# Kernel optimization log

Hardware: AMD Instinct MI355X
Metric: run time of the kernel (lower is better)

The kernel has to match this reference:

```python
import jax, jax.numpy as jnp
import numpy as np

# nqsystems=8 grouped sites, physical dim d=2^ncontraq=16,
# state bond r=64, layer (unitary MPO) bond rl=16, operator MPO bond ro=4,
# nlsystems=1 pre-contracted circuit layer.
NQ, R, D, RL, RO, NL = 8, 64, 16, 16, 4, 1


def setup_inputs() -> dict:
    key = jax.random.key(0)
    k1, k2, k3 = jax.random.split(key, 3)
    # scale so contractions stay O(1) numerically
    state = jax.random.normal(k1, (NQ, R, D, R), jnp.float32) / np.float32(np.sqrt(R * D))
    layer = jax.random.normal(k2, (NL, NQ, RL, D, D, RL), jnp.float32) / np.float32(np.sqrt(RL * D))
    operator = jax.random.normal(k3, (NQ, RO, D, D, RO), jnp.float32) / np.float32(np.sqrt(RO * D))
    return {"state": state, "layer": layer, "operator": operator}


def reference(state, layer, operator):
    """<psi| U^dagger O U |psi> contracted site-by-site along the TT chain.

    state:    [nq, r, d, r]        TT cores of |psi>
    layer:    [nl, nq, rl, d, d, rl]  TT-operator cores of the circuit layer (nl=1)
    operator: [nq, ro, d, d, ro]   TT-operator cores of the observable
    """
    r, rl, ro = state.shape[1], layer.shape[3], operator.shape[1]
    # open-boundary closure: boundary vectors = e0 on every bond
    env0 = jnp.zeros((r, rl, ro, rl, r), state.dtype).at[0, 0, 0, 0, 0].set(1.0)
    U = layer[0]  # nlsystems == 1

    def step(env, cores):
        S, Uq, Oq = cores
        # tt_dagger: conj + transpose physical indices (0,2,1,3)
        Ud = jnp.conj(Uq).transpose(0, 2, 1, 3)
        # env axes: a=bra-state bond, l=bra-layer bond, o=operator bond,
        #           m=ket-layer bond, b=ket-state bond
        t = jnp.einsum('alomb,aiA->lombiA', env, jnp.conj(S))   # bra state core
        t = jnp.einsum('lombiA,lijL->ombAjL', t, Ud)            # U^dagger core
        t = jnp.einsum('ombAjL,ojkO->mbALkO', t, Oq)            # observable core
        t = jnp.einsum('mbALkO,mksM->bALOsM', t, Uq)            # U core
        t = jnp.einsum('bALOsM,bsB->ALOMB', t, S)               # ket state core
        return t, None

    env, _ = jax.lax.scan(step, env0, (state, U, operator))
    return env[0, 0, 0, 0, 0]
```

## Files before the change

kernel.cpp:

```cpp
#include <hip/hip_runtime.h>


typedef __attribute__((ext_vector_type(8))) short bf16x8;
typedef __attribute__((ext_vector_type(8))) _Float16 f16x8;
typedef __attribute__((ext_vector_type(4))) float f32x4;
typedef __attribute__((ext_vector_type(4))) unsigned short us4;

static __device__ __forceinline__ unsigned short f2bf(float x) {
    union { float f; unsigned u; } a; a.f = x;
    return (unsigned short)((a.u + 0x7FFF + ((a.u >> 16) & 1)) >> 16);
}
static __device__ __forceinline__ float bf2f(unsigned short h) {
    union { unsigned u; float f; } a; a.u = (unsigned)h << 16; return a.f;
}
static __device__ __forceinline__ unsigned split2(float x) {
    unsigned short h = f2bf(x);
    unsigned short l = f2bf(x - bf2f(h));
    return (unsigned)h | ((unsigned)l << 16);
}
static __device__ __forceinline__ void split2_pair(float x0, float x1,
                                                   unsigned& o0, unsigned& o1) {
    unsigned hh, ll;
    asm("v_cvt_pk_bf16_f32 %0, %1, %2" : "=v"(hh) : "v"(x0), "v"(x1));
    union { unsigned u; float f; } c0, c1;
    c0.u = hh << 16;
    c1.u = hh & 0xffff0000u;
    float r0 = x0 - c0.f, r1 = x1 - c1.f;
    asm("v_cvt_pk_bf16_f32 %0, %1, %2" : "=v"(ll) : "v"(r0), "v"(r1));
    asm("v_perm_b32 %0, %1, %2, %3" : "=v"(o0) : "v"(ll), "v"(hh), "s"(0x05040100));
    asm("v_perm_b32 %0, %1, %2, %3" : "=v"(o1) : "v"(ll), "v"(hh), "s"(0x07060302));
}
static __device__ __forceinline__ unsigned short f2h_bits(float x) {
    union { _Float16 h; unsigned short u; } c; c.h = (_Float16)x; return c.u;
}
static __device__ __forceinline__ float h2f_bits(unsigned short u) {
    union { unsigned short u; _Float16 h; } c; c.u = u; return (float)c.h;
}
static __device__ __forceinline__ void gl_lds16(const unsigned short* g,
                                                unsigned short* l) {
    __builtin_amdgcn_global_load_lds(
        (const __attribute__((address_space(1))) unsigned int*)g,
        (__attribute__((address_space(3))) unsigned int*)l, 16, 0, 0);
}

__global__ void write_diag_kernel(float* out, float v) {
    if (threadIdx.x == 0 && blockIdx.x == 0) out[0] = v;
}
__global__ void zero_out(float* o) {
    if (threadIdx.x == 0 && blockIdx.x == 0) o[0] = 0.0f;
}

__global__ void prep_apack(const float* __restrict__ layer,
                           unsigned short* __restrict__ Ap2,
                           unsigned short* __restrict__ Ap4) {
    int idx = blockIdx.x * 256 + threadIdx.x;
    int q = idx >> 13, k0 = (idx >> 10) & 7, mt = (idx >> 6) & 15, lane = idx & 63;
    int quad = lane >> 4, r = lane & 15;
    unsigned short h2[8], l2[8], h4[8], l4[8];
#pragma unroll
    for (int j = 0; j < 8; j++) {
        int k = k0 * 32 + quad * 8 + j;
        int m = mt * 16 + r;
        float v2 = layer[(size_t)q * 65536 +
                         (size_t)((((k >> 4) * 16 + (m >> 4)) * 16 + (k & 15)) * 16 + (m & 15))];
        float v4 = layer[(size_t)q * 65536 +
                         (size_t)((((k >> 4) * 16 + (k & 15)) * 16 + (m >> 4)) * 16 + (m & 15))];
        h2[j] = f2h_bits(v2); l2[j] = f2h_bits(v2 - h2f_bits(h2[j]));
        h4[j] = f2h_bits(v4); l4[j] = f2h_bits(v4 - h2f_bits(h4[j]));
    }
    size_t base = ((size_t)((q * 8 + k0) * 16 + mt) * 2) * 512 + lane * 8;
    *(us4*)(Ap2 + base)       = *(us4*)&h2[0];
    *(us4*)(Ap2 + base + 4)   = *(us4*)&h2[4];
    *(us4*)(Ap2 + base + 512) = *(us4*)&l2[0];
    *(us4*)(Ap2 + base + 516) = *(us4*)&l2[4];
    *(us4*)(Ap4 + base)       = *(us4*)&h4[0];
    *(us4*)(Ap4 + base + 4)   = *(us4*)&h4[4];
    *(us4*)(Ap4 + base + 512) = *(us4*)&l4[0];
    *(us4*)(Ap4 + base + 516) = *(us4*)&l4[4];
}

__global__ void prep_spack1(const float* __restrict__ state,
                            unsigned short* __restrict__ Sp1) {
    int idx = blockIdx.x * 256 + threadIdx.x;
    int q = idx >> 13, c = (idx >> 11) & 3, k0 = (idx >> 10) & 1,
        mt = (idx >> 6) & 15, lane = idx & 63;
    int quad = lane >> 4, lr = lane & 15;
    unsigned short h[8], l[8];
#pragma unroll
    for (int j = 0; j < 8; j++) {
        int k = k0 * 32 + quad * 8 + j;
        float v = state[(size_t)q * 65536 + (size_t)(k * 16 + mt) * 64 + c * 16 + lr];
        h[j] = f2bf(v); l[j] = f2bf(v - bf2f(h[j]));
    }
    size_t base = (size_t)(q * 4 + c) * 32768 + ((size_t)(k0 * 16 + mt) * 2) * 512 + lane * 8;
    *(us4*)(Sp1 + base)       = *(us4*)&h[0];
    *(us4*)(Sp1 + base + 4)   = *(us4*)&h[4];
    *(us4*)(Sp1 + base + 512) = *(us4*)&l[0];
    *(us4*)(Sp1 + base + 516) = *(us4*)&l[4];
}

__global__ void prep_spack5(const float* __restrict__ state,
                            unsigned short* __restrict__ Sp5) {
    int idx = blockIdx.x * 256 + threadIdx.x;
    int q = idx >> 13, k0 = (idx >> 8) & 31, mt = (idx >> 6) & 3, lane = idx & 63;
    int quad = lane >> 4, lr = lane & 15;
    unsigned short h[8], l[8];
#pragma unroll
    for (int j = 0; j < 8; j++) {
        int k = k0 * 32 + quad * 8 + j;
        int s = k >> 6, b = k & 63;
        float v = state[(size_t)q * 65536 + (size_t)(b * 16 + s) * 64 + mt * 16 + lr];
        h[j] = f2bf(v); l[j] = f2bf(v - bf2f(h[j]));
    }
    size_t base = (size_t)q * 131072 + ((size_t)(k0 * 4 + mt) * 2) * 512 + lane * 8;
    *(us4*)(Sp5 + base)       = *(us4*)&h[0];
    *(us4*)(Sp5 + base + 4)   = *(us4*)&h[4];
    *(us4*)(Sp5 + base + 512) = *(us4*)&l[0];
    *(us4*)(Sp5 + base + 516) = *(us4*)&l[4];
}

__global__ void prep_opack3(const float* __restrict__ oper,
                            unsigned short* __restrict__ Op3) {
    int idx = blockIdx.x * 256 + threadIdx.x;
    int q = idx >> 9, k0 = (idx >> 8) & 1, mt = (idx >> 6) & 3, lane = idx & 63;
    int quad = lane >> 4, lr = lane & 15;
    unsigned short h[8], l[8];
#pragma unroll
    for (int j = 0; j < 8; j++) {
        int k = k0 * 32 + quad * 8 + j;
        int m = mt * 16 + lr;
        float v = oper[(size_t)q * 4096 + (size_t)(k * 16 + (m & 15)) * 4 + (m >> 4)];
        h[j] = f2h_bits(v); l[j] = f2h_bits(v - h2f_bits(h[j]));
    }
    size_t base = (size_t)q * 8192 + ((size_t)(k0 * 4 + mt) * 2) * 512 + lane * 8;
    *(us4*)(Op3 + base)       = *(us4*)&h[0];
    *(us4*)(Op3 + base + 4)   = *(us4*)&h[4];
    *(us4*)(Op3 + base + 512) = *(us4*)&l[0];
    *(us4*)(Op3 + base + 516) = *(us4*)&l[4];
}

__global__ void env_split_k(const float* __restrict__ env, unsigned* __restrict__ envS) {
    int t = blockIdx.x * 256 + threadIdx.x;
    float4 v = ((const float4*)env)[t];
    uint4 o;
    o.x = split2(v.x); o.y = split2(v.y); o.z = split2(v.z); o.w = split2(v.w);
    ((uint4*)envS)[t] = o;
}

__global__ void s0_g2(const float* __restrict__ state, const float* __restrict__ layer,
                      float* __restrict__ g2) {
    int t = blockIdx.x * 256 + threadIdx.x;
    int A = t >> 8, j = (t >> 4) & 15, L = t & 15;
    float s = 0;
    for (int i = 0; i < 16; i++) s += state[i * 64 + A] * layer[(j * 16 + i) * 16 + L];
    g2[t] = s;
}
__global__ void s0_g3(const float* __restrict__ g2, const float* __restrict__ oper,
                      float* __restrict__ g3) {
    int t = blockIdx.x * 256 + threadIdx.x;
    int A = t >> 10, L = (t >> 6) & 15, k = (t >> 2) & 15, O = t & 3;
    float s = 0;
    for (int j = 0; j < 16; j++) s += g2[A * 256 + j * 16 + L] * oper[(j * 16 + k) * 4 + O];
    g3[t] = s;
}
__global__ void s0_g4(const float* __restrict__ g3, const float* __restrict__ layer,
                      float* __restrict__ g4) {
    int t = blockIdx.x * 256 + threadIdx.x;
    int A = t >> 14, L = (t >> 10) & 15, O = (t >> 8) & 3, sp = (t >> 4) & 15, M = t & 15;
    float s = 0;
    for (int k = 0; k < 16; k++)
        s += g3[A * 1024 + L * 64 + k * 4 + O] * layer[(k * 16 + sp) * 16 + M];
    g4[t] = s;
}
__global__ void s0_env(const float* __restrict__ g4, const float* __restrict__ state,
                       float* __restrict__ env) {
    int t = blockIdx.x * 256 + threadIdx.x;
    int A = t >> 16, L = (t >> 12) & 15, O = (t >> 10) & 3, M = (t >> 6) & 15, B = t & 63;
    float s = 0;
    for (int sp = 0; sp < 16; sp++)
        s += g4[A * 16384 + L * 1024 + O * 256 + sp * 16 + M] * state[sp * 64 + B];
    env[(size_t)(L * 64 + O * 16 + M) * 4096 + A * 64 + B] = s;
}

__global__ void s7_c1(const float* __restrict__ state, const float* __restrict__ layer,
                      float* __restrict__ c1) {
    int t = blockIdx.x * 256 + threadIdx.x;
    int l = t >> 10, a = (t >> 4) & 63, j = t & 15;
    float s = 0;
    for (int i = 0; i < 16; i++)
        s += state[7 * 65536 + (a * 16 + i) * 64] * layer[7 * 65536 + ((l * 16 + j) * 16 + i) * 16];
    c1[t] = s;
}
__global__ void s7_c2(const float* __restrict__ c1, const float* __restrict__ oper,
                      float* __restrict__ c2) {
    int t = blockIdx.x * 256 + threadIdx.x;
    int o = t >> 14, l = (t >> 10) & 15, a = (t >> 4) & 63, k = t & 15;
    float s = 0;
    for (int j = 0; j < 16; j++)
        s += c1[l * 1024 + a * 16 + j] * oper[7 * 4096 + ((o * 16 + j) * 16 + k) * 4];
    c2[t] = s;
}
__global__ void s7_c3(const float* __restrict__ c2, const float* __restrict__ layer,
                      float* __restrict__ c3) {
    int t = blockIdx.x * 256 + threadIdx.x;
    int m = t >> 16, o = (t >> 14) & 3, l = (t >> 10) & 15, a = (t >> 4) & 63, sp = t & 15;
    float s = 0;
    for (int k = 0; k < 16; k++)
        s += c2[o * 16384 + l * 1024 + a * 16 + k] *
             layer[7 * 65536 + ((m * 16 + k) * 16 + sp) * 16];
    c3[t] = s;
}
__global__ void prep_sv(const float* __restrict__ state, float* __restrict__ sv) {
    int t = blockIdx.x * 256 + threadIdx.x;
    sv[t] = state[7 * 65536 + t * 64];
}
__global__ __launch_bounds__(256) void s7_fused(const float* __restrict__ env,
                                                const float* __restrict__ c3,
                                                const float* __restrict__ sv,
                                                float* __restrict__ out) {
    __shared__ float c3s[1024], svs[1024], red[256];
    int t = threadIdx.x;
    int n0 = blockIdx.x * 64;
    int l = n0 >> 12, o = (n0 >> 10) & 3, m = (n0 >> 6) & 15;
    const float* c3b = c3 + m * 65536 + o * 16384 + l * 1024;
    const float* eb  = env + (size_t)blockIdx.x * 4096;
    for (int i = t; i < 1024; i += 256) { c3s[i] = c3b[i]; svs[i] = sv[i]; }
    __syncthreads();
    float s = 0;
    int b = t & 63, ag = t >> 6;
#pragma unroll
    for (int g = 0; g < 16; g++) {
        int a = ag * 16 + g;
        float e = eb[a * 64 + b];
        float w = 0;
#pragma unroll
        for (int sp = 0; sp < 16; sp++) w += c3s[a * 16 + sp] * svs[b * 16 + sp];
        s += e * w;
    }
    red[t] = s; __syncthreads();
    for (int off = 128; off; off >>= 1) { if (t < off) red[t] += red[t + off]; __syncthreads(); }
    if (t == 0) atomicAdd(out, red[0]);
}

static __device__ __forceinline__ void g1_body(int bid, void* smem,
                                               const unsigned* __restrict__ envS,
                                               const unsigned short* __restrict__ Sp1,
                                               unsigned short* __restrict__ t1,
                                               float scale) {
    unsigned* Bt = (unsigned*)smem;
    const int tid = threadIdx.x, lane = tid & 63, wave = tid >> 6;
    const int quad = lane >> 4, lr = lane & 15;
    const int cc = bid >> 10, rid = bid & 1023;
    const int l = rid >> 6, o = (rid >> 4) & 3, m2 = rid & 15;

    f32x4 acc[4][4];
#pragma unroll
    for (int i = 0; i < 4; i++)
#pragma unroll
        for (int j = 0; j < 4; j++)
#pragma unroll
            for (int r = 0; r < 4; r++) acc[i][j][r] = 0.0f;

    const unsigned* Bv = envS + (size_t)rid * 4096;
    const unsigned short* Sp1c = Sp1 + (size_t)cc * 32768;
    uint4 ur[2];
    auto load_tile = [&](int k0) {
        const uint4* src = (const uint4*)(Bv + k0 * 2048);
        ur[0] = src[tid];
        ur[1] = src[256 + tid];
    };
    auto store_tile = [&]() {
#pragma unroll
        for (int v = 0; v < 2; v++) {
            int e = v * 256 + tid;
            unsigned* p = &Bt[(e >> 4) * 65 + (e & 15) * 4];
            p[0] = ur[v].x; p[1] = ur[v].y; p[2] = ur[v].z; p[3] = ur[v].w;
        }
    };

    bf16x8 ahb[2][4], alb[2][4];
    auto loadA = [&](int k0, int buf) {
#pragma unroll
        for (int mt = 0; mt < 4; mt++) {
            int gmt = wave * 4 + mt;
            const unsigned short* ap = Sp1c + ((size_t)(k0 * 16 + gmt) * 2) * 512 + lane * 8;
            ahb[buf][mt] = *(const bf16x8*)ap;
            alb[buf][mt] = *(const bf16x8*)(ap + 512);
        }
    };

    load_tile(0);
    loadA(0, 0);
    store_tile();
#pragma unroll
    for (int k0 = 0; k0 < 2; k0++) {
        __syncthreads();
        if (k0 + 1 < 2) { load_tile(k0 + 1); loadA(k0 + 1, 1); }
#pragma unroll
        for (int nt = 0; nt < 4; nt++) {
            int nl = nt * 16 + lr;
            bf16x8 bh, bl;
#pragma unroll
            for (int j = 0; j < 8; j++) {
                unsigned u = Bt[(quad * 8 + j) * 65 + nl];
                bh[j] = (short)(u & 0xffffu);
                bl[j] = (short)(u >> 16);
            }
#pragma unroll
            for (int mt = 0; mt < 4; mt++) {
                acc[mt][nt] = __builtin_amdgcn_mfma_f32_16x16x32_bf16(ahb[k0][mt], bh, acc[mt][nt], 0, 0, 0);
                acc[mt][nt] = __builtin_amdgcn_mfma_f32_16x16x32_bf16(ahb[k0][mt], bl, acc[mt][nt], 0, 0, 0);
                acc[mt][nt] = __builtin_amdgcn_mfma_f32_16x16x32_bf16(alb[k0][mt], bh, acc[mt][nt], 0, 0, 0);
            }
        }
        __syncthreads();
        if (k0 + 1 < 2) store_tile();
    }

#pragma unroll
    for (int nt = 0; nt < 4; nt++) {
        int b = nt * 16 + lr;
#pragma unroll
        for (int r = 0; r < 4; r++) {
            int a4 = quad * 4 + r;
            us4 w;
#pragma unroll
            for (int mt = 0; mt < 4; mt++) w[mt] = f2h_bits(acc[mt][nt][r] * scale);
            size_t addr = (size_t)cc * 16777216 +
                          (size_t)(o * 256 + m2 * 16 + a4) * 16384 +
                          (size_t)(l * 2 + (wave >> 1)) * 512 + b * 8 + (wave & 1) * 4;
            *(us4*)(t1 + addr) = w;
        }
    }
}

__global__ __launch_bounds__(256) void gemm_g1(const unsigned* __restrict__ envS,
                                               const unsigned short* __restrict__ Sp1,
                                               unsigned short* __restrict__ t1,
                                               float scale) {
    __shared__ unsigned Bt[32 * 65];
    g1_body(blockIdx.x, Bt, envS, Sp1, t1, scale);
}

static __device__ __forceinline__ void g2_body(int bid, void* smem,
                                               const unsigned short* __restrict__ Bp,
                                               const unsigned short* __restrict__ Ap,
                                               unsigned short* __restrict__ Co) {
    unsigned short* Bs = (unsigned short*)smem;
    const int tid = threadIdx.x, lane = tid & 63, wave = tid >> 6;
    const int quad = lane >> 4, lr = lane & 15;
    const int cc = bid >> 10, rid = bid & 1023;
    const int o = rid >> 8, m2 = (rid >> 4) & 15, a4 = rid & 15;
    const unsigned short* pb = Bp + (size_t)bid * 16384;
    unsigned short* Cb = Co + (size_t)cc * 16777216;

#pragma unroll
    for (int i = 0; i < 8; i++)
        gl_lds16(pb + i * 2048 + tid * 8, Bs + i * 2048 + wave * 512);

    f32x4 acc[4][4];
#pragma unroll
    for (int i = 0; i < 4; i++)
#pragma unroll
        for (int j = 0; j < 4; j++)
#pragma unroll
            for (int r = 0; r < 4; r++) acc[i][j][r] = 0.0f;

    f16x8 ah[3][4];
    auto loadA = [&](int k0, int buf) {
#pragma unroll
        for (int mt = 0; mt < 4; mt++) {
            int gmt = wave * 4 + mt;
            ah[buf][mt] = *(const f16x8*)(Ap + ((size_t)(k0 * 16 + gmt) * 2) * 512 + lane * 8);
        }
    };
    loadA(0, 0);
    loadA(1, 1);

    asm volatile("s_waitcnt vmcnt(0)" ::: "memory");
    __syncthreads();

#pragma unroll
    for (int k0 = 0; k0 < 8; k0++) {
        if (k0 + 2 < 8) loadA(k0 + 2, (k0 + 2) % 3);
        f16x8 bfr[4];
#pragma unroll
        for (int nt = 0; nt < 4; nt++)
            bfr[nt] = *(const f16x8*)(Bs + (k0 * 4 + quad) * 512 + (nt * 16 + lr) * 8);
#pragma unroll
        for (int nt = 0; nt < 4; nt++)
#pragma unroll
            for (int mt = 0; mt < 4; mt++)
                acc[mt][nt] = __builtin_amdgcn_mfma_f32_16x16x32_f16(
                    ah[k0 % 3][mt], bfr[nt], acc[mt][nt], 0, 0, 0);
    }

#pragma unroll
    for (int nt = 0; nt < 4; nt++) {
        int b = nt * 16 + lr;
#pragma unroll
        for (int r = 0; r < 4; r++) {
            int L = quad * 4 + r;
            us4 w;
#pragma unroll
            for (int mt = 0; mt < 4; mt++) w[mt] = f2h_bits(acc[mt][nt][r]);
            size_t addr = (size_t)(L * 256 + m2 * 16 + a4) * 4096 +
                          (size_t)(o * 2 + (wave >> 1)) * 512 + b * 8 + (wave & 1) * 4;
            *(us4*)(Cb + addr) = w;
        }
    }
}

__global__ __launch_bounds__(256) void gemm_g2(const unsigned short* __restrict__ Bp,
                                               const unsigned short* __restrict__ Ap,
                                               unsigned short* __restrict__ Co) {
    __shared__ __align__(16) unsigned short Bs[16384];
    g2_body(blockIdx.x, Bs, Bp, Ap, Co);
}

__global__ __launch_bounds__(256) void gemm_g45(const unsigned short* __restrict__ T2,
                                                const unsigned short* __restrict__ Op3q,
                                                const unsigned short* __restrict__ Ap4,
                                                const unsigned short* __restrict__ Sp5,
                                                float* __restrict__ env,
                                                unsigned* __restrict__ envSo,
                                                int A0, float inv, int wf32) {
    __shared__ __align__(16) unsigned short Bs[16384];
    __shared__ unsigned SL[4 * 16 * 68];
    const int tid = threadIdx.x, lane = tid & 63, wave = tid >> 6;
    const int quad = lane >> 4, lr = lane & 15;
    const int cc = blockIdx.x >> 10, rid = blockIdx.x & 1023;
    const int low = rid & 7, O2 = (rid >> 3) & 3, g = rid >> 5;
    const int panel = g * 8 + low;
    const int L = panel >> 4, a4 = panel & 15;
    const unsigned short* T2c = T2 + (size_t)cc * 16777216;
    const int b8 = (wave * 16 + lr) * 8;

    f16x8 ah[3][4];
    auto loadA = [&](int k0, int buf) {
#pragma unroll
        for (int mt = 0; mt < 4; mt++) {
            int gmt = wave * 4 + mt;
            ah[buf][mt] = *(const f16x8*)(Ap4 + ((size_t)(k0 * 16 + gmt) * 2) * 512 + lane * 8);
        }
    };
    loadA(0, 0);
    loadA(1, 1);

    {
        f16x8 oh0 = *(const f16x8*)(Op3q + (size_t)(O2 * 2) * 512 + lane * 8);
        f16x8 oh1 = *(const f16x8*)(Op3q + (size_t)((4 + O2) * 2) * 512 + lane * 8);
        f16x8 tb[5][2];
        auto loadT2 = [&](int m2, int buf) {
            const unsigned short* pp = T2c + (size_t)(L * 256 + m2 * 16 + a4) * 4096;
            tb[buf][0] = *(const f16x8*)(pp + (quad << 9) + b8);
            tb[buf][1] = *(const f16x8*)(pp + ((4 + quad) << 9) + b8);
        };
        loadT2(0, 0); loadT2(1, 1); loadT2(2, 2); loadT2(3, 3);
#pragma unroll
        for (int m2 = 0; m2 < 16; m2++) {
            if (m2 + 4 < 16) loadT2(m2 + 4, (m2 + 4) % 5);
            f32x4 a3;
            a3[0] = a3[1] = a3[2] = a3[3] = 0.0f;
            a3 = __builtin_amdgcn_mfma_f32_16x16x32_f16(oh0, tb[m2 % 5][0], a3, 0, 0, 0);
            a3 = __builtin_amdgcn_mfma_f32_16x16x32_f16(oh1, tb[m2 % 5][1], a3, 0, 0, 0);
            us4 w;
#pragma unroll
            for (int r = 0; r < 4; r++) w[r] = f2h_bits(a3[r]);
            *(us4*)(Bs + (m2 * 2 + (quad >> 1)) * 512 + b8 + (quad & 1) * 4) = w;
        }
    }
    __syncthreads();

    f32x4 acc[4][4];
#pragma unroll
    for (int i = 0; i < 4; i++)
#pragma unroll
        for (int j = 0; j < 4; j++)
#pragma unroll
            for (int r = 0; r < 4; r++) acc[i][j][r] = 0.0f;

#pragma unroll
    for (int k0 = 0; k0 < 8; k0++) {
        if (k0 + 2 < 8) loadA(k0 + 2, (k0 + 2) % 3);
        f16x8 bfr[4];
#pragma unroll
        for (int nt = 0; nt < 4; nt++)
            bfr[nt] = *(const f16x8*)(Bs + (k0 * 4 + quad) * 512 + (nt * 16 + lr) * 8);
#pragma unroll
        for (int nt = 0; nt < 4; nt++)
#pragma unroll
            for (int mt = 0; mt < 4; mt++)
                acc[mt][nt] = __builtin_amdgcn_mfma_f32_16x16x32_f16(
                    ah[k0 % 3][mt], bfr[nt], acc[mt][nt], 0, 0, 0);
    }

    unsigned* myslab = SL + wave * (16 * 68);
    f32x4 acc5[4];
#pragma unroll
    for (int nt = 0; nt < 4; nt++)
#pragma unroll
        for (int r = 0; r < 4; r++) acc5[nt][r] = 0.0f;

    bf16x8 s5h[2][4], s5l[2][4];
    auto loadS5 = [&](int step, int buf) {
        int kg = (wave * 4 + (step >> 1)) * 2 + (step & 1);
#pragma unroll
        for (int nt = 0; nt < 4; nt++) {
            const unsigned short* bp = Sp5 + ((size_t)(kg * 4 + nt) * 2) * 512 + lane * 8;
            s5h[buf][nt] = *(const bf16x8*)bp;
            s5l[buf][nt] = *(const bf16x8*)(bp + 512);
        }
    };
    loadS5(0, 0);

#pragma unroll
    for (int mtp = 0; mtp < 4; mtp++) {
#pragma unroll
        for (int nt = 0; nt < 4; nt++) {
            unsigned o0, o1, o2, o3;
            split2_pair(acc[mtp][nt][0], acc[mtp][nt][1], o0, o1);
            split2_pair(acc[mtp][nt][2], acc[mtp][nt][3], o2, o3);
            myslab[(quad * 4 + 0) * 68 + nt * 16 + lr] = o0;
            myslab[(quad * 4 + 1) * 68 + nt * 16 + lr] = o1;
            myslab[(quad * 4 + 2) * 68 + nt * 16 + lr] = o2;
            myslab[(quad * 4 + 3) * 68 + nt * 16 + lr] = o3;
        }
        asm volatile("s_waitcnt lgkmcnt(0)" ::: "memory");
#pragma unroll
        for (int h = 0; h < 2; h++) {
            const int step = mtp * 2 + h;
            const unsigned* sp = &myslab[lr * 68 + h * 32 + quad * 8];
            uint4 u0 = *(const uint4*)sp;
            uint4 u1 = *(const uint4*)(sp + 4);
            bf16x8 th, tl;
            th[0] = (short)(u0.x & 0xffff); tl[0] = (short)(u0.x >> 16);
            th[1] = (short)(u0.y & 0xffff); tl[1] = (short)(u0.y >> 16);
            th[2] = (short)(u0.z & 0xffff); tl[2] = (short)(u0.z >> 16);
            th[3] = (short)(u0.w & 0xffff); tl[3] = (short)(u0.w >> 16);
            th[4] = (short)(u1.x & 0xffff); tl[4] = (short)(u1.x >> 16);
            th[5] = (short)(u1.y & 0xffff); tl[5] = (short)(u1.y >> 16);
            th[6] = (short)(u1.z & 0xffff); tl[6] = (short)(u1.z >> 16);
            th[7] = (short)(u1.w & 0xffff); tl[7] = (short)(u1.w >> 16);
            if (step + 1 < 8) loadS5(step + 1, (step + 1) & 1);
#pragma unroll
            for (int nt = 0; nt < 4; nt++) {
                acc5[nt] = __builtin_amdgcn_mfma_f32_16x16x32_bf16(th, s5h[step & 1][nt], acc5[nt], 0, 0, 0);
                acc5[nt] = __builtin_amdgcn_mfma_f32_16x16x32_bf16(th, s5l[step & 1][nt], acc5[nt], 0, 0, 0);
                acc5[nt] = __builtin_amdgcn_mfma_f32_16x16x32_bf16(tl, s5h[step & 1][nt], acc5[nt], 0, 0, 0);
            }
        }
    }

    __syncthreads();
    float* red = (float*)SL;
#pragma unroll
    for (int nt = 0; nt < 4; nt++)
#pragma unroll
        for (int r = 0; r < 4; r++)
            red[wave * 1088 + (quad * 4 + r) * 68 + nt * 16 + lr] = acc5[nt][r];
    __syncthreads();
    float wv[4];
#pragma unroll
    for (int r = 0; r < 4; r++) {
        int M2 = quad * 4 + r, Bc = wave * 16 + lr;
        float v = red[M2 * 68 + Bc] + red[1088 + M2 * 68 + Bc] +
                  red[2176 + M2 * 68 + Bc] + red[3264 + M2 * 68 + Bc];
        wv[r] = v * inv;
    }
    unsigned s0p, s1p, s2p, s3p;
    split2_pair(wv[0], wv[1], s0p, s1p);
    split2_pair(wv[2], wv[3], s2p, s3p);
    unsigned sp4[4] = {s0p, s1p, s2p, s3p};
#pragma unroll
    for (int r = 0; r < 4; r++) {
        int M2 = quad * 4 + r, Bc = wave * 16 + lr;
        size_t idx = (size_t)(L * 64 + O2 * 16 + M2) * 4096 + (A0 + cc * 16 + a4) * 64 + Bc;
        envSo[idx] = sp4[r];
        if (wf32) env[idx] = wv[r];
    }
}

__global__ __launch_bounds__(256) void fused_g2_g1(
        const unsigned short* __restrict__ Bp,
        const unsigned short* __restrict__ Ap,
        unsigned short* __restrict__ Co,
        const unsigned* __restrict__ envS,
        const unsigned short* __restrict__ Sp1b,
        unsigned short* __restrict__ t1,
        float scale) {
    __shared__ __align__(16) unsigned char smem[32768];
    const int grp = blockIdx.x >> 3;
    const int sub = (grp >> 1) * 8 + (blockIdx.x & 7);
    if (grp & 1)
        g1_body(sub, smem, envS, Sp1b, t1, scale);
    else
        g2_body(sub, smem, Bp, Ap, Co);
}

extern "C" void kernel_launch(void* const* d_in, const int* in_sizes, int n_in,
                              void* d_out, int out_size, void* d_ws, size_t ws_size,
                              hipStream_t stream) {
    const float* state = (const float*)d_in[0];
    const float* layer = (const float*)d_in[1];
    const float* oper  = (const float*)d_in[2];
    float* out = (float*)d_out;

    const size_t need = 16777216ull * 4 + 33554432ull * 4 + 3ull * 4194304ull * 4 +
                        (4ull * 1048576ull + 65536ull) * 2ull + 4096ull;
    if (ws_size < need) {
        write_diag_kernel<<<1, 64, 0, stream>>>(out, (float)ws_size);
        return;
    }
    float* F    = (float*)d_ws;
    unsigned* P = (unsigned*)(F + 16777216);
    unsigned* envS0 = (unsigned*)(P + 33554432);
    float* envB = (float*)(envS0 + 4194304);
    unsigned* envS1 = (unsigned*)(envB + 4194304);
    unsigned short* Ap2 = (unsigned short*)(envS1 + 4194304);
    unsigned short* Ap4 = Ap2 + 1048576;
    unsigned short* Sp1 = Ap4 + 1048576;
    unsigned short* Sp5 = Sp1 + 1048576;
    unsigned short* Op3 = Sp5 + 1048576;
    float* sv = (float*)(Op3 + 65536);
    float* SCR = F;
    unsigned short* T1p0 = (unsigned short*)P;
    unsigned short* T1p1 = T1p0 + 33554432;
    unsigned short* T2p0 = (unsigned short*)F;
    unsigned short* T2p1 = T1p0;

    prep_apack<<<256, 256, 0, stream>>>(layer, Ap2, Ap4);
    prep_spack1<<<256, 256, 0, stream>>>(state, Sp1);
    prep_spack5<<<256, 256, 0, stream>>>(state, Sp5);
    prep_opack3<<<16, 256, 0, stream>>>(oper, Op3);
    prep_sv<<<4, 256, 0, stream>>>(state, sv);

    s0_g2<<<64, 256, 0, stream>>>(state, layer, SCR);
    s0_g3<<<256, 256, 0, stream>>>(SCR, oper, SCR + 16384);
    s0_g4<<<4096, 256, 0, stream>>>(SCR + 16384, layer, SCR + 81920);
    s0_env<<<16384, 256, 0, stream>>>(SCR + 81920, state, envB);
    env_split_k<<<4096, 256, 0, stream>>>(envB, envS1);

    for (int q = 1; q < 7; q++) {
        unsigned* einS  = (q & 1) ? envS1 : envS0;
        unsigned* eoutS = (q & 1) ? envS0 : envS1;
        float scl = (float)(1u << (16 + 2 * q));
        float inv = 1.0f / scl;
        int wf32 = (q == 6) ? 1 : 0;
        gemm_g1<<<2048, 256, 0, stream>>>(
            einS, Sp1 + (size_t)(q * 4 + 0) * 32768, T1p0, scl);
        fused_g2_g1<<<4096, 256, 0, stream>>>(
            T1p0, Ap2 + (size_t)q * 131072, T2p0,
            einS, Sp1 + (size_t)(q * 4 + 2) * 32768, T1p1, scl);
        gemm_g45<<<2048, 256, 0, stream>>>(
            T2p0, Op3 + (size_t)q * 8192, Ap4 + (size_t)q * 131072,
            Sp5 + (size_t)q * 131072, envB, eoutS, 0, inv, wf32);
        gemm_g2<<<2048, 256, 0, stream>>>(
            T1p1, Ap2 + (size_t)q * 131072, T2p1);
        gemm_g45<<<2048, 256, 0, stream>>>(
            T2p1, Op3 + (size_t)q * 8192, Ap4 + (size_t)q * 131072,
            Sp5 + (size_t)q * 131072, envB, eoutS, 32, inv, wf32);
    }

    s7_c1<<<64, 256, 0, stream>>>(state, layer, SCR);
    s7_c2<<<256, 256, 0, stream>>>(SCR, oper, SCR + 16384);
    s7_c3<<<4096, 256, 0, stream>>>(SCR + 16384, layer, SCR + 81920);
    zero_out<<<1, 64, 0, stream>>>(out);
    s7_fused<<<1024, 256, 0, stream>>>(envB, SCR + 81920, sv, out);
}
```

Measured before the change: 1.385 ms.

## Split gemm_g45 work across eight waves and alias shared buffers

Doubles gemm_g45 from 256 to 512 threads. Each wave now handles half the M tiles in the main GEMM, half the m2 slices in the operator stage, and half the output columns in the final split-bf16 GEMM. The Bs staging buffer is aliased onto the slab array, so shared memory per block stays near the old size despite the extra waves. The cost is more __syncthreads barriers, a full slab write pass before the last GEMM (it was previously interleaved per wave), and a larger cross-wave reduction.

```diff
diff --git a/kernel.cpp b/kernel.cpp
--- a/kernel.cpp
+++ b/kernel.cpp
@@ -418,15 +418,15 @@
     g2_body(blockIdx.x, Bs, Bp, Ap, Co);
 }
 
-__global__ __launch_bounds__(256) void gemm_g45(const unsigned short* __restrict__ T2,
+__global__ __launch_bounds__(512) void gemm_g45(const unsigned short* __restrict__ T2,
                                                 const unsigned short* __restrict__ Op3q,
                                                 const unsigned short* __restrict__ Ap4,
                                                 const unsigned short* __restrict__ Sp5,
                                                 float* __restrict__ env,
                                                 unsigned* __restrict__ envSo,
                                                 int A0, float inv, int wf32) {
-    __shared__ __align__(16) unsigned short Bs[16384];
-    __shared__ unsigned SL[4 * 16 * 68];
+    __shared__ __align__(16) unsigned SL[16 * 1088];
+    unsigned short* Bs = (unsigned short*)SL;
     const int tid = threadIdx.x, lane = tid & 63, wave = tid >> 6;
     const int quad = lane >> 4, lr = lane & 15;
     const int cc = blockIdx.x >> 10, rid = blockIdx.x & 1023;
@@ -434,13 +434,14 @@
     const int panel = g * 8 + low;
     const int L = panel >> 4, a4 = panel & 15;
     const unsigned short* T2c = T2 + (size_t)cc * 16777216;
-    const int b8 = (wave * 16 + lr) * 8;
-
-    f16x8 ah[3][4];
+    const int bw = wave & 3, mh = wave >> 2;
+    const int b8 = (bw * 16 + lr) * 8;
+
+    f16x8 ah[3][2];
     auto loadA = [&](int k0, int buf) {
 #pragma unroll
-        for (int mt = 0; mt < 4; mt++) {
-            int gmt = wave * 4 + mt;
+        for (int mt = 0; mt < 2; mt++) {
+            int gmt = wave * 2 + mt;
             ah[buf][mt] = *(const f16x8*)(Ap4 + ((size_t)(k0 * 16 + gmt) * 2) * 512 + lane * 8);
         }
     };
@@ -450,20 +451,21 @@
     {
         f16x8 oh0 = *(const f16x8*)(Op3q + (size_t)(O2 * 2) * 512 + lane * 8);
         f16x8 oh1 = *(const f16x8*)(Op3q + (size_t)((4 + O2) * 2) * 512 + lane * 8);
-        f16x8 tb[5][2];
+        f16x8 tb[3][2];
         auto loadT2 = [&](int m2, int buf) {
             const unsigned short* pp = T2c + (size_t)(L * 256 + m2 * 16 + a4) * 4096;
             tb[buf][0] = *(const f16x8*)(pp + (quad << 9) + b8);
             tb[buf][1] = *(const f16x8*)(pp + ((4 + quad) << 9) + b8);
         };
-        loadT2(0, 0); loadT2(1, 1); loadT2(2, 2); loadT2(3, 3);
-#pragma unroll
-        for (int m2 = 0; m2 < 16; m2++) {
-            if (m2 + 4 < 16) loadT2(m2 + 4, (m2 + 4) % 5);
+        loadT2(mh * 8 + 0, 0); loadT2(mh * 8 + 1, 1);
+#pragma unroll
+        for (int i = 0; i < 8; i++) {
+            int m2 = mh * 8 + i;
+            if (i + 2 < 8) loadT2(mh * 8 + i + 2, (i + 2) % 3);
             f32x4 a3;
             a3[0] = a3[1] = a3[2] = a3[3] = 0.0f;
-            a3 = __builtin_amdgcn_mfma_f32_16x16x32_f16(oh0, tb[m2 % 5][0], a3, 0, 0, 0);
-            a3 = __builtin_amdgcn_mfma_f32_16x16x32_f16(oh1, tb[m2 % 5][1], a3, 0, 0, 0);
+            a3 = __builtin_amdgcn_mfma_f32_16x16x32_f16(oh0, tb[i % 3][0], a3, 0, 0, 0);
+            a3 = __builtin_amdgcn_mfma_f32_16x16x32_f16(oh1, tb[i % 3][1], a3, 0, 0, 0);
             us4 w;
 #pragma unroll
             for (int r = 0; r < 4; r++) w[r] = f2h_bits(a3[r]);
@@ -472,9 +474,9 @@
     }
     __syncthreads();
 
-    f32x4 acc[4][4];
-#pragma unroll
-    for (int i = 0; i < 4; i++)
+    f32x4 acc[2][4];
+#pragma unroll
+    for (int i = 0; i < 2; i++)
 #pragma unroll
         for (int j = 0; j < 4; j++)
 #pragma unroll
@@ -490,94 +492,103 @@
 #pragma unroll
         for (int nt = 0; nt < 4; nt++)
 #pragma unroll
-            for (int mt = 0; mt < 4; mt++)
+            for (int mt = 0; mt < 2; mt++)
                 acc[mt][nt] = __builtin_amdgcn_mfma_f32_16x16x32_f16(
                     ah[k0 % 3][mt], bfr[nt], acc[mt][nt], 0, 0, 0);
     }
 
-    unsigned* myslab = SL + wave * (16 * 68);
-    f32x4 acc5[4];
-#pragma unroll
-    for (int nt = 0; nt < 4; nt++)
-#pragma unroll
-        for (int r = 0; r < 4; r++) acc5[nt][r] = 0.0f;
-
-    bf16x8 s5h[2][4], s5l[2][4];
-    auto loadS5 = [&](int step, int buf) {
-        int kg = (wave * 4 + (step >> 1)) * 2 + (step & 1);
+    __syncthreads();
+
+#pragma unroll
+    for (int mt = 0; mt < 2; mt++) {
+        unsigned* slab = SL + (wave * 2 + mt) * 1088;
 #pragma unroll
         for (int nt = 0; nt < 4; nt++) {
+            unsigned o0, o1, o2, o3;
+            split2_pair(acc[mt][nt][0], acc[mt][nt][1], o0, o1);
+            split2_pair(acc[mt][nt][2], acc[mt][nt][3], o2, o3);
+            slab[(quad * 4 + 0) * 68 + nt * 16 + lr] = o0;
+            slab[(quad * 4 + 1) * 68 + nt * 16 + lr] = o1;
+            slab[(quad * 4 + 2) * 68 + nt * 16 + lr] = o2;
+            slab[(quad * 4 + 3) * 68 + nt * 16 + lr] = o3;
+        }
+    }
+    __syncthreads();
+
+    const int v = wave >> 1, hp = wave & 1;
+    f32x4 acc5[2];
+#pragma unroll
+    for (int j = 0; j < 2; j++)
+#pragma unroll
+        for (int r = 0; r < 4; r++) acc5[j][r] = 0.0f;
+
+    bf16x8 s5h[2][2], s5l[2][2];
+    auto loadS5 = [&](int st, int buf) {
+        int kg = (4 * v + (st >> 1)) * 2 + (st & 1);
+#pragma unroll
+        for (int j = 0; j < 2; j++) {
+            int nt = hp * 2 + j;
             const unsigned short* bp = Sp5 + ((size_t)(kg * 4 + nt) * 2) * 512 + lane * 8;
-            s5h[buf][nt] = *(const bf16x8*)bp;
-            s5l[buf][nt] = *(const bf16x8*)(bp + 512);
+            s5h[buf][j] = *(const bf16x8*)bp;
+            s5l[buf][j] = *(const bf16x8*)(bp + 512);
         }
     };
     loadS5(0, 0);
 
 #pragma unroll
-    for (int mtp = 0; mtp < 4; mtp++) {
-#pragma unroll
-        for (int nt = 0; nt < 4; nt++) {
-            unsigned o0, o1, o2, o3;
-            split2_pair(acc[mtp][nt][0], acc[mtp][nt][1], o0, o1);
-            split2_pair(acc[mtp][nt][2], acc[mtp][nt][3], o2, o3);
-            myslab[(quad * 4 + 0) * 68 + nt * 16 + lr] = o0;
-            myslab[(quad * 4 + 1) * 68 + nt * 16 + lr] = o1;
-            myslab[(quad * 4 + 2) * 68 + nt * 16 + lr] = o2;
-            myslab[(quad * 4 + 3) * 68 + nt * 16 + lr] = o3;
-        }
-        asm volatile("s_waitcnt lgkmcnt(0)" ::: "memory");
-#pragma unroll
-        for (int h = 0; h < 2; h++) {
-            const int step = mtp * 2 + h;
-            const unsigned* sp = &myslab[lr * 68 + h * 32 + quad * 8];
-            uint4 u0 = *(const uint4*)sp;
-            uint4 u1 = *(const uint4*)(sp + 4);
-            bf16x8 th, tl;
-            th[0] = (short)(u0.x & 0xffff); tl[0] = (short)(u0.x >> 16);
-            th[1] = (short)(u0.y & 0xffff); tl[1] = (short)(u0.y >> 16);
-            th[2] = (short)(u0.z & 0xffff); tl[2] = (short)(u0.z >> 16);
-            th[3] = (short)(u0.w & 0xffff); tl[3] = (short)(u0.w >> 16);
-            th[4] = (short)(u1.x & 0xffff); tl[4] = (short)(u1.x >> 16);
-            th[5] = (short)(u1.y & 0xffff); tl[5] = (short)(u1.y >> 16);
-            th[6] = (short)(u1.z & 0xffff); tl[6] = (short)(u1.z >> 16);
-            th[7] = (short)(u1.w & 0xffff); tl[7] = (short)(u1.w >> 16);
-            if (step + 1 < 8) loadS5(step + 1, (step + 1) & 1);
-#pragma unroll
-            for (int nt = 0; nt < 4; nt++) {
-                acc5[nt] = __builtin_amdgcn_mfma_f32_16x16x32_bf16(th, s5h[step & 1][nt], acc5[nt], 0, 0, 0);
-                acc5[nt] = __builtin_amdgcn_mfma_f32_16x16x32_bf16(th, s5l[step & 1][nt], acc5[nt], 0, 0, 0);
-                acc5[nt] = __builtin_amdgcn_mfma_f32_16x16x32_bf16(tl, s5h[step & 1][nt], acc5[nt], 0, 0, 0);
-            }
+    for (int st = 0; st < 8; st++) {
+        const int s = 4 * v + (st >> 1), h = st & 1;
+        const unsigned* sp = SL + s * 1088 + lr * 68 + h * 32 + quad * 8;
+        uint4 u0 = *(const uint4*)sp;
+        uint4 u1 = *(const uint4*)(sp + 4);
+        bf16x8 th, tl;
+        th[0] = (short)(u0.x & 0xffff); tl[0] = (short)(u0.x >> 16);
+        th[1] = (short)(u0.y & 0xffff); tl[1] = (short)(u0.y >> 16);
+        th[2] = (short)(u0.z & 0xffff); tl[2] = (short)(u0.z >> 16);
+        th[3] = (short)(u0.w & 0xffff); tl[3] = (short)(u0.w >> 16);
+        th[4] = (short)(u1.x & 0xffff); tl[4] = (short)(u1.x >> 16);
+        th[5] = (short)(u1.y & 0xffff); tl[5] = (short)(u1.y >> 16);
+        th[6] = (short)(u1.z & 0xffff); tl[6] = (short)(u1.z >> 16);
+        th[7] = (short)(u1.w & 0xffff); tl[7] = (short)(u1.w >> 16);
+        if (st + 1 < 8) loadS5(st + 1, (st + 1) & 1);
+#pragma unroll
+        for (int j = 0; j < 2; j++) {
+            acc5[j] = __builtin_amdgcn_mfma_f32_16x16x32_bf16(th, s5h[st & 1][j], acc5[j], 0, 0, 0);
+            acc5[j] = __builtin_amdgcn_mfma_f32_16x16x32_bf16(th, s5l[st & 1][j], acc5[j], 0, 0, 0);
+            acc5[j] = __builtin_amdgcn_mfma_f32_16x16x32_bf16(tl, s5h[st & 1][j], acc5[j], 0, 0, 0);
         }
     }
 
     __syncthreads();
     float* red = (float*)SL;
 #pragma unroll
-    for (int nt = 0; nt < 4; nt++)
+    for (int j = 0; j < 2; j++)
 #pragma unroll
         for (int r = 0; r < 4; r++)
-            red[wave * 1088 + (quad * 4 + r) * 68 + nt * 16 + lr] = acc5[nt][r];
+            red[wave * 1088 + (quad * 4 + r) * 68 + (hp * 2 + j) * 16 + lr] = acc5[j][r];
     __syncthreads();
-    float wv[4];
-#pragma unroll
-    for (int r = 0; r < 4; r++) {
-        int M2 = quad * 4 + r, Bc = wave * 16 + lr;
-        float v = red[M2 * 68 + Bc] + red[1088 + M2 * 68 + Bc] +
-                  red[2176 + M2 * 68 + Bc] + red[3264 + M2 * 68 + Bc];
-        wv[r] = v * inv;
-    }
-    unsigned s0p, s1p, s2p, s3p;
-    split2_pair(wv[0], wv[1], s0p, s1p);
-    split2_pair(wv[2], wv[3], s2p, s3p);
-    unsigned sp4[4] = {s0p, s1p, s2p, s3p};
-#pragma unroll
-    for (int r = 0; r < 4; r++) {
-        int M2 = quad * 4 + r, Bc = wave * 16 + lr;
+
+    const int ntl = v & 1, rp = v >> 1;
+    const int Bc = hp * 32 + ntl * 16 + lr;
+    float wv[2];
+#pragma unroll
+    for (int rr = 0; rr < 2; rr++) {
+        int M2 = quad * 4 + rp * 2 + rr;
+        float val = red[(0 + hp) * 1088 + M2 * 68 + Bc] +
+                    red[(2 + hp) * 1088 + M2 * 68 + Bc] +
+                    red[(4 + hp) * 1088 + M2 * 68 + Bc] +
+                    red[(6 + hp) * 1088 + M2 * 68 + Bc];
+        wv[rr] = val * inv;
+    }
+    unsigned p0, p1;
+    split2_pair(wv[0], wv[1], p0, p1);
+    unsigned pq[2] = {p0, p1};
+#pragma unroll
+    for (int rr = 0; rr < 2; rr++) {
+        int M2 = quad * 4 + rp * 2 + rr;
         size_t idx = (size_t)(L * 64 + O2 * 16 + M2) * 4096 + (A0 + cc * 16 + a4) * 64 + Bc;
-        envSo[idx] = sp4[r];
-        if (wf32) env[idx] = wv[r];
+        envSo[idx] = pq[rr];
+        if (wf32) env[idx] = wv[rr];
     }
 }
 
@@ -652,12 +663,12 @@
         fused_g2_g1<<<4096, 256, 0, stream>>>(
             T1p0, Ap2 + (size_t)q * 131072, T2p0,
             einS, Sp1 + (size_t)(q * 4 + 2) * 32768, T1p1, scl);
-        gemm_g45<<<2048, 256, 0, stream>>>(
+        gemm_g45<<<2048, 512, 0, stream>>>(
             T2p0, Op3 + (size_t)q * 8192, Ap4 + (size_t)q * 131072,
             Sp5 + (size_t)q * 131072, envB, eoutS, 0, inv, wf32);
         gemm_g2<<<2048, 256, 0, stream>>>(
             T1p1, Ap2 + (size_t)q * 131072, T2p1);
-        gemm_g45<<<2048, 256, 0, stream>>>(
+        gemm_g45<<<2048, 512, 0, stream>>>(
             T2p1, Op3 + (size_t)q * 8192, Ap4 + (size_t)q * 131072,
             Sp5 + (size_t)q * 131072, envB, eoutS, 32, inv, wf32);
     }
```

Result: no change. 1.407 ms (+1.6%).
